# Performance work log

Measured on AMD Instinct MI355X. Metric: run time of the kernel, lower is better.

## Reference

```python
import jax, jax.numpy as jnp
import numpy as np

K = 8  # knn_graph(k=8, loop=True): self-loop kept, so self is among the k nearest


def knn_idx(x, k):
    # x: [N, F]. Pairwise squared distances via the expansion trick.
    x2 = jnp.sum(x * x, axis=-1)                      # [N]
    d = x2[:, None] + x2[None, :] - 2.0 * (x @ x.T)   # [N, N]
    _, idx = jax.lax.top_k(-d, k)                     # [N, k] nearest (incl. self)
    return idx


def edge_conv(x, idx, W1, b1, W2, b2):
    # PyG EdgeConv: message = nn(cat([x_i, x_j - x_i])), aggr='max'.
    # Every node has exactly k incoming edges, so scatter-max == max over the k axis.
    n, f = x.shape
    k = idx.shape[1]
    xi = x[:, None, :]                                # [N, 1, F] center
    xj = x[idx]                                       # [N, k, F] neighbors (gather)
    e = jnp.concatenate([jnp.broadcast_to(xi, (n, k, f)), xj - xi], axis=-1)  # [N,k,2F]
    h = jax.nn.relu(e @ W1 + b1) @ W2 + b2            # [N, k, out]
    return jnp.max(h, axis=1)                         # [N, out]


def setup_inputs() -> dict:
    key = jax.random.key(0)
    ks = jax.random.split(key, 9)
    B, N, F = 2, 4096, 3
    H0, H1, OUT = 64, 128, 256

    def lin(kw, fan_in, fan_out):
        bound = 1.0 / np.sqrt(fan_in)
        kw1, kw2 = jax.random.split(kw)
        W = jax.random.uniform(kw1, (fan_in, fan_out), jnp.float32, -bound, bound)
        b = jax.random.uniform(kw2, (fan_out,), jnp.float32, -bound, bound)
        return W, b

    W1, b1 = lin(ks[0], 2 * F, H0)
    W2, b2 = lin(ks[1], H0, H1)
    W3, b3 = lin(ks[2], 2 * H1, H1)
    W4, b4 = lin(ks[3], H1, OUT)
    point_cloud = jax.random.normal(ks[4], (B, N, F), jnp.float32)
    return {"point_cloud": point_cloud, "W1": W1, "b1": b1, "W2": W2, "b2": b2,
            "W3": W3, "b3": b3, "W4": W4, "b4": b4}


def reference(point_cloud, W1, b1, W2, b2, W3, b3, W4, b4):
    B, N, F = point_cloud.shape
    pts = point_cloud.reshape(B * N, F)               # knn over ALL B*N points (no batch vec)
    idx = knn_idx(jax.lax.stop_gradient(pts), K)      # [B*N, K]
    x = jax.nn.relu(edge_conv(pts, idx, W1, b1, W2, b2))
    x = edge_conv(x, idx, W3, b3, W4, b4)
    return x.reshape(B, N, -1)
```

## Files before the change

kernel.cpp:

```cpp
#include <hip/hip_runtime.h>

#define NPTS 8192
#define NSLICE 64
#define SLICE_LEN (NPTS / NSLICE)
#define KNN 8
#define SURV_CAP 48
#define TQ 32

typedef short bf16x8 __attribute__((ext_vector_type(8)));
typedef float f32x4 __attribute__((ext_vector_type(4)));

__device__ __forceinline__ unsigned short f2bf(float x) {
  unsigned int u = __float_as_uint(x);
  return (unsigned short)((u + 0x7FFF + ((u >> 16) & 1)) >> 16);
}
__device__ __forceinline__ float bf2f(unsigned short s) {
  return __uint_as_float(((unsigned int)s) << 16);
}

__device__ __forceinline__ float dist_exact(float qx, float qy, float qz,
                                            float q2, float px, float py,
                                            float pz, float p2) {
#pragma clang fp contract(off)
  float dot = __fmaf_rn(qz, pz, __fmaf_rn(qy, py, __fmul_rn(qx, px)));
  float t1 = __fadd_rn(q2, p2);
  return __fadd_rn(t1, __fmul_rn(-2.0f, dot));
}

__device__ __forceinline__ float norm2_exact(float x, float y, float z) {
#pragma clang fp contract(off)
  return __fadd_rn(__fadd_rn(__fmul_rn(x, x), __fmul_rn(y, y)),
                   __fmul_rn(z, z));
}

__device__ __forceinline__ float med3(float a, float b, float c) {
  return __builtin_amdgcn_fmed3f(a, b, c);
}

__device__ __forceinline__ double pack_key(float d, int idx) {
  unsigned int ub = __float_as_uint(d);
  ub ^= (((unsigned int)((int)ub >> 31)) | 0x80000000u);
  unsigned int lo = (ub << 13) | (unsigned int)idx;
  unsigned int hi = 0x3ff00000u | (ub >> 19);
  return __hiloint2double((int)hi, (int)lo);
}

#define KEY_DECL                                                            \
  const double KINF = __longlong_as_double(0x7ff0000000000000LL);           \
  double k0 = KINF, k1 = KINF, k2 = KINF, k3 = KINF, k4 = KINF, k5 = KINF,  \
         k6 = KINF, k7 = KINF;
#define KB1(s)                                                              \
  {                                                                         \
    double mn = fmin(carry, k##s);                                          \
    carry = fmax(carry, k##s);                                              \
    k##s = mn;                                                              \
  }
#define KEY_INSERT(key)                                                     \
  {                                                                         \
    double carry = (key);                                                   \
    KB1(0) KB1(1) KB1(2) KB1(3) KB1(4) KB1(5) KB1(6) KB1(7)                 \
  }

#define VINS(dv)                                                            \
  {                                                                         \
    float dd = (dv);                                                        \
    v7 = med3(dd, v6, v7);                                                  \
    v6 = med3(dd, v5, v6);                                                  \
    v5 = med3(dd, v4, v5);                                                  \
    v4 = med3(dd, v3, v4);                                                  \
    v3 = med3(dd, v2, v2 < dd ? dd : v3);                                   \
    v2 = med3(dd, v1, v2);                                                  \
    v1 = med3(dd, v0, v1);                                                  \
    v0 = fminf(dd, v0);                                                     \
  }

#undef VINS
#define VINS(dv)                                                            \
  {                                                                         \
    float dd = (dv);                                                        \
    v7 = med3(dd, v6, v7);                                                  \
    v6 = med3(dd, v5, v6);                                                  \
    v5 = med3(dd, v4, v5);                                                  \
    v4 = med3(dd, v3, v4);                                                  \
    v3 = med3(dd, v2, v3);                                                  \
    v2 = med3(dd, v1, v2);                                                  \
    v1 = med3(dd, v0, v1);                                                  \
    v0 = fminf(dd, v0);                                                     \
  }

#define VDECL                                                               \
  const float FINF = __uint_as_float(0x7f800000u);                          \
  float v0 = FINF, v1 = FINF, v2 = FINF, v3 = FINF, v4 = FINF, v5 = FINF,   \
        v6 = FINF, v7 = FINF;

#define VINS2(dv)                                                           \
  {                                                                         \
    float dd = (dv);                                                        \
    s1 = med3(dd, s0, s1);                                                  \
    s0 = fminf(dd, s0);                                                     \
  }

__global__ __launch_bounds__(256) void prep_kernel(
    const float* __restrict__ W4, const float* __restrict__ pts,
    unsigned short* __restrict__ W4ht, unsigned short* __restrict__ W4lt,
    float4* __restrict__ pts4) {
  const int id = blockIdx.x * 256 + threadIdx.x;
  const int k = id >> 8, c = id & 255;
  float v = W4[k * 256 + c];
  unsigned short hi = f2bf(v);
  unsigned short lo = f2bf(v - bf2f(hi));
  W4ht[c * 128 + k] = hi;
  W4lt[c * 128 + k] = lo;
  if (id < NPTS) {
    float x = pts[id * 3 + 0];
    float y = pts[id * 3 + 1];
    float z = pts[id * 3 + 2];
    pts4[id] = make_float4(x, y, z, norm2_exact(x, y, z));
  }
}

__global__ __launch_bounds__(256) void knn_vals_kernel(
    const float4* __restrict__ pts4, float* __restrict__ part_v) {
  __shared__ float4 sp[SLICE_LEN];
  const int t = threadIdx.x;
  const int q = blockIdx.x * 256 + t;
  const int jbase = blockIdx.y * SLICE_LEN;
  for (int p = t; p < SLICE_LEN; p += 256) sp[p] = pts4[jbase + p];
  __syncthreads();
  const float4 qp = pts4[q];
  const float qx = qp.x, qy = qp.y, qz = qp.z, q2 = qp.w;
  const float FINF = __uint_as_float(0x7f800000u);
  float s0 = FINF, s1 = FINF;
  for (int p = 0; p < SLICE_LEN; p += 8) {
    float4 c0 = sp[p + 0];
    float4 c1 = sp[p + 1];
    float4 c2 = sp[p + 2];
    float4 c3 = sp[p + 3];
    float4 c4 = sp[p + 4];
    float4 c5 = sp[p + 5];
    float4 c6 = sp[p + 6];
    float4 c7 = sp[p + 7];
    float d0 = dist_exact(qx, qy, qz, q2, c0.x, c0.y, c0.z, c0.w);
    float d1 = dist_exact(qx, qy, qz, q2, c1.x, c1.y, c1.z, c1.w);
    float d2 = dist_exact(qx, qy, qz, q2, c2.x, c2.y, c2.z, c2.w);
    float d3 = dist_exact(qx, qy, qz, q2, c3.x, c3.y, c3.z, c3.w);
    float d4 = dist_exact(qx, qy, qz, q2, c4.x, c4.y, c4.z, c4.w);
    float d5 = dist_exact(qx, qy, qz, q2, c5.x, c5.y, c5.z, c5.w);
    float d6 = dist_exact(qx, qy, qz, q2, c6.x, c6.y, c6.z, c6.w);
    float d7 = dist_exact(qx, qy, qz, q2, c7.x, c7.y, c7.z, c7.w);
    VINS2(d0);
    VINS2(d1);
    VINS2(d2);
    VINS2(d3);
    VINS2(d4);
    VINS2(d5);
    VINS2(d6);
    VINS2(d7);
  }
  float* o = &part_v[(size_t)(blockIdx.y * 2) * NPTS + q];
  o[0 * NPTS] = s0;
  o[1 * NPTS] = s1;
}

__global__ __launch_bounds__(256) void knn_thresh_kernel(
    const float* __restrict__ part_v, float* __restrict__ thr,
    unsigned long long* __restrict__ mask) {
  __shared__ float v8s[TQ][8][9];
  __shared__ float smin[TQ][65];
  const int t = threadIdx.x;
  const int lq = t >> 3, c = t & 7;
  const int q = blockIdx.x * TQ + lq;
  {
    VDECL;
#pragma unroll
    for (int s8 = 0; s8 < 8; ++s8) {
      const int s = c * 8 + s8;
      const float* col = &part_v[(size_t)(s * 2) * NPTS + q];
      float a0 = col[0 * (size_t)NPTS];
      float a1 = col[1 * (size_t)NPTS];
      smin[lq][s] = a0;
      VINS(a0);
      VINS(a1);
    }
    v8s[lq][c][0] = v0;
    v8s[lq][c][1] = v1;
    v8s[lq][c][2] = v2;
    v8s[lq][c][3] = v3;
    v8s[lq][c][4] = v4;
    v8s[lq][c][5] = v5;
    v8s[lq][c][6] = v6;
    v8s[lq][c][7] = v7;
  }
  __syncthreads();
  if (c == 0) {
    VDECL;
#pragma unroll
    for (int s = 0; s < 8; ++s) {
      VINS(v8s[lq][s][0]);
      VINS(v8s[lq][s][1]);
      VINS(v8s[lq][s][2]);
      VINS(v8s[lq][s][3]);
      VINS(v8s[lq][s][4]);
      VINS(v8s[lq][s][5]);
      VINS(v8s[lq][s][6]);
      VINS(v8s[lq][s][7]);
    }
    const float tcol = v7 + fabsf(v7) * 4e-5f + 1e-20f;
    const float tmask = v7 + fabsf(v7) * 8e-5f + 2e-20f;
    unsigned long long mk = 0;
#pragma unroll
    for (int s = 0; s < NSLICE; ++s) {
      if (smin[lq][s] <= tmask) mk |= (1ull << s);
    }
    thr[q] = tcol;
    mask[q] = mk;
  }
}

__global__ __launch_bounds__(256) void knn_collect_kernel(
    const float4* __restrict__ pts4, const float* __restrict__ thr,
    const unsigned long long* __restrict__ mask, int* __restrict__ nbr) {
  __shared__ double keybuf[4][SURV_CAP];
  __shared__ int scnt[4];
  const int t = threadIdx.x;
  const int wv = t >> 6;
  const int lane = t & 63;
  const int q = blockIdx.x * 4 + wv;
  if (lane == 0) scnt[wv] = 0;
  __syncthreads();
  const float4 qp = pts4[q];
  const float qx = qp.x, qy = qp.y, qz = qp.z, q2 = qp.w;
  const float thrq = thr[q];
  unsigned long long m = mask[q];
  while (m) {
    const int s = (int)__ffsll(m) - 1;
    m &= m - 1;
    const int base = s * SLICE_LEN;
#pragma unroll
    for (int r = 0; r < SLICE_LEN / 64; ++r) {
      const int j = base + r * 64 + lane;
      const float4 cp = pts4[j];
      const float d = dist_exact(qx, qy, qz, q2, cp.x, cp.y, cp.z, cp.w);
      if (d <= thrq) {
        int slot = atomicAdd(&scnt[wv], 1);
        if (slot < SURV_CAP) keybuf[wv][slot] = pack_key(d, j);
      }
    }
  }
  __syncthreads();
  if (lane == 0) {
    int c = scnt[wv];
    if (c > SURV_CAP) c = SURV_CAP;
    KEY_DECL;
    for (int u = 0; u < c; ++u) {
      KEY_INSERT(keybuf[wv][u]);
    }
    int* o = &nbr[q * KNN];
    o[0] = __double2loint(k0) & 0x1fff;
    o[1] = __double2loint(k1) & 0x1fff;
    o[2] = __double2loint(k2) & 0x1fff;
    o[3] = __double2loint(k3) & 0x1fff;
    o[4] = __double2loint(k4) & 0x1fff;
    o[5] = __double2loint(k5) & 0x1fff;
    o[6] = __double2loint(k6) & 0x1fff;
    o[7] = __double2loint(k7) & 0x1fff;
  }
}

__global__ __launch_bounds__(256) void gemm1_fused_kernel(
    const float* __restrict__ pts, const int* __restrict__ nbr,
    const float* __restrict__ W1, const float* __restrict__ b1,
    const float* __restrict__ W2, const float* __restrict__ b2,
    float* __restrict__ y) {
  __shared__ float es[64][6];
  __shared__ float W1s[6][64];
  __shared__ float b1s[64];
  __shared__ float As[64][64];
  __shared__ float Bs[64][64];
  const int t = threadIdx.x;
  const int rowBase = blockIdx.y * 64;
  const int colBase = blockIdx.x * 64;

  for (int idx = t; idx < 384; idx += 256) W1s[idx >> 6][idx & 63] = W1[idx];
  if (t < 64) b1s[t] = b1[t];
  {
    int cq = t & 15, kr = t >> 4;
#pragma unroll
    for (int it = 0; it < 4; ++it) {
      int k = it * 16 + kr;
      *(float4*)&Bs[k][cq * 4] =
          *(const float4*)&W2[(size_t)k * 128 + colBase + cq * 4];
    }
  }
  if (t < 64) {
    int e = rowBase + t;
    int i = e >> 3;
    int j = nbr[e];
    float xi0 = pts[i * 3], xi1 = pts[i * 3 + 1], xi2 = pts[i * 3 + 2];
    es[t][0] = xi0;
    es[t][1] = xi1;
    es[t][2] = xi2;
    es[t][3] = pts[j * 3] - xi0;
    es[t][4] = pts[j * 3 + 1] - xi1;
    es[t][5] = pts[j * 3 + 2] - xi2;
  }
  __syncthreads();

  {
    const int e = t & 63, k0 = (t >> 6) * 16;
    const float f0 = es[e][0], f1 = es[e][1], f2 = es[e][2];
    const float f3 = es[e][3], f4 = es[e][4], f5 = es[e][5];
#pragma unroll
    for (int k = 0; k < 16; ++k) {
      int c = k0 + k;
      float v = b1s[c];
      v = fmaf(f0, W1s[0][c], v);
      v = fmaf(f1, W1s[1][c], v);
      v = fmaf(f2, W1s[2][c], v);
      v = fmaf(f3, W1s[3][c], v);
      v = fmaf(f4, W1s[4][c], v);
      v = fmaf(f5, W1s[5][c], v);
      As[c][e] = fmaxf(v, 0.0f);
    }
  }
  __syncthreads();

  const int tx = t & 15, ty = t >> 4;
  float acc[4][4] = {};
#pragma unroll 8
  for (int k = 0; k < 64; ++k) {
    float4 a = *(const float4*)&As[k][ty * 4];
    float4 b = *(const float4*)&Bs[k][tx * 4];
    const float ar[4] = {a.x, a.y, a.z, a.w};
    const float br[4] = {b.x, b.y, b.z, b.w};
#pragma unroll
    for (int i = 0; i < 4; ++i)
#pragma unroll
      for (int jj = 0; jj < 4; ++jj)
        acc[i][jj] = fmaf(ar[i], br[jj], acc[i][jj]);
  }
  __syncthreads();

  float* Mx = &As[0][0];
#pragma unroll
  for (int jj = 0; jj < 4; ++jj) {
    float m =
        fmaxf(fmaxf(acc[0][jj], acc[1][jj]), fmaxf(acc[2][jj], acc[3][jj]));
    Mx[ty * 64 + tx * 4 + jj] = m;
  }
  __syncthreads();
  if (t < 128) {
    int p = t >> 4, cq = t & 15;
    int c = cq * 4;
    float4 o;
    float* oa = (float*)&o;
#pragma unroll
    for (int jj = 0; jj < 4; ++jj) {
      float v = fmaxf(Mx[(2 * p) * 64 + c + jj], Mx[(2 * p + 1) * 64 + c + jj]);
      v += b2[colBase + c + jj];
      oa[jj] = fmaxf(v, 0.0f);
    }
    *(float4*)&y[(size_t)(blockIdx.y * 8 + p) * 128 + colBase + c] = o;
  }
}

__global__ __launch_bounds__(256) void gemm_ac_kernel(
    const float* __restrict__ A, const float* __restrict__ W3,
    const float* __restrict__ bias, float* __restrict__ out) {
  __shared__ float As[64][64];
  __shared__ float Bs[64][64];
  const int t = threadIdx.x;
  const int tx = t & 15, ty = t >> 4;
  const int rowBase = blockIdx.y * 64;
  const int colBase = blockIdx.x * 64;
  const float4* A4 = (const float4*)A;
  float acc[4][4] = {};
  const int K = 128, Nglob = 256;

  for (int k0 = 0; k0 < K; k0 += 64) {
#pragma unroll
    for (int it = 0; it < 4; ++it) {
      int idx = it * 256 + t;
      int row = idx & 63, kq = idx >> 6;
      float4 av = A4[(size_t)(rowBase + row) * (K >> 2) + (k0 >> 2) + kq];
      As[kq * 4 + 0][row] = av.x;
      As[kq * 4 + 1][row] = av.y;
      As[kq * 4 + 2][row] = av.z;
      As[kq * 4 + 3][row] = av.w;
    }
#pragma unroll
    for (int it = 0; it < 4; ++it) {
      int idx = it * 256 + t;
      int cq = idx & 15, kr = idx >> 4;
      const float* src =
          (colBase < 128)
              ? &W3[(size_t)(k0 + kr) * 128 + colBase]
              : &W3[(size_t)(128 + k0 + kr) * 128 + (colBase - 128)];
      float4 bv = *(const float4*)&src[cq * 4];
      *(float4*)&Bs[kr][cq * 4] = bv;
    }
    __syncthreads();
#pragma unroll 8
    for (int k = 0; k < 64; ++k) {
      float4 a = *(const float4*)&As[k][ty * 4];
      float4 b = *(const float4*)&Bs[k][tx * 4];
      const float ar[4] = {a.x, a.y, a.z, a.w};
      const float br[4] = {b.x, b.y, b.z, b.w};
#pragma unroll
      for (int i = 0; i < 4; ++i)
#pragma unroll
        for (int jj = 0; jj < 4; ++jj)
          acc[i][jj] = fmaf(ar[i], br[jj], acc[i][jj]);
    }
    __syncthreads();
  }

#pragma unroll
  for (int i = 0; i < 4; ++i) {
    float4 o;
    float* oa = (float*)&o;
#pragma unroll
    for (int jj = 0; jj < 4; ++jj) {
      float v = acc[i][jj];
      int cg = colBase + tx * 4 + jj;
      if (cg < 128) v += bias[cg];
      oa[jj] = v;
    }
    *(float4*)&out[(size_t)(rowBase + ty * 4 + i) * Nglob + colBase + tx * 4] =
        o;
  }
}

__global__ __launch_bounds__(256) void gemm2_mfma_kernel(
    const float* __restrict__ AC, const int* __restrict__ nbr,
    const unsigned short* __restrict__ W4ht,
    const unsigned short* __restrict__ W4lt, const float* __restrict__ b4,
    float* __restrict__ out) {
  __shared__ unsigned short H2h[128 * 40];
  __shared__ unsigned short H2l[128 * 40];
  __shared__ unsigned short Wth[128 * 40];
  __shared__ unsigned short Wtl[128 * 40];
  const int t = threadIdx.x;
  const int rowBase = blockIdx.y * 128;
  const int colBase = blockIdx.x * 128;
  const int eloc = t >> 1, hh = t & 1;
  const int kb = hh * 16;
  const int edge = rowBase + eloc;
  const int ip = edge >> 3;
  const int jp = nbr[edge];
  const float* ai_p = AC + (size_t)ip * 256;
  const float* ci_p = ai_p + 128;
  const float* cj_p = AC + (size_t)jp * 256 + 128;
  const int lane = t & 63;
  const int w = t >> 6;
  const int q = lane >> 4;
  const int nidx = lane & 15;

  f32x4 acc[2][8];
#pragma unroll
  for (int mt = 0; mt < 2; ++mt)
#pragma unroll
    for (int nt = 0; nt < 8; ++nt) acc[mt][nt] = (f32x4){0.f, 0.f, 0.f, 0.f};

  for (int p = 0; p < 4; ++p) {
    const int k0 = p * 32;
    {
      float h2[16];
      const float4* a4 = (const float4*)(ai_p + k0 + kb);
      const float4* c4 = (const float4*)(ci_p + k0 + kb);
      const float4* d4 = (const float4*)(cj_p + k0 + kb);
#pragma unroll
      for (int u = 0; u < 4; ++u) {
        float4 a = a4[u], c = c4[u], d = d4[u];
        h2[u * 4 + 0] = fmaxf(a.x + d.x - c.x, 0.f);
        h2[u * 4 + 1] = fmaxf(a.y + d.y - c.y, 0.f);
        h2[u * 4 + 2] = fmaxf(a.z + d.z - c.z, 0.f);
        h2[u * 4 + 3] = fmaxf(a.w + d.w - c.w, 0.f);
      }
      unsigned int hp[8], lp[8];
#pragma unroll
      for (int u = 0; u < 8; ++u) {
        unsigned short h0 = f2bf(h2[2 * u]), h1 = f2bf(h2[2 * u + 1]);
        hp[u] = (unsigned int)h0 | ((unsigned int)h1 << 16);
        unsigned short l0 = f2bf(h2[2 * u] - bf2f(h0));
        unsigned short l1 = f2bf(h2[2 * u + 1] - bf2f(h1));
        lp[u] = (unsigned int)l0 | ((unsigned int)l1 << 16);
      }
      *(uint4*)&H2h[eloc * 40 + kb] = make_uint4(hp[0], hp[1], hp[2], hp[3]);
      *(uint4*)&H2h[eloc * 40 + kb + 8] =
          make_uint4(hp[4], hp[5], hp[6], hp[7]);
      *(uint4*)&H2l[eloc * 40 + kb] = make_uint4(lp[0], lp[1], lp[2], lp[3]);
      *(uint4*)&H2l[eloc * 40 + kb + 8] =
          make_uint4(lp[4], lp[5], lp[6], lp[7]);
    }
    {
      const size_t src = (size_t)(colBase + eloc) * 128 + k0 + kb;
      *(uint4*)&Wth[eloc * 40 + kb] = *(const uint4*)&W4ht[src];
      *(uint4*)&Wth[eloc * 40 + kb + 8] = *(const uint4*)&W4ht[src + 8];
      *(uint4*)&Wtl[eloc * 40 + kb] = *(const uint4*)&W4lt[src];
      *(uint4*)&Wtl[eloc * 40 + kb + 8] = *(const uint4*)&W4lt[src + 8];
    }
    __syncthreads();
    bf16x8 ah[2], al[2];
#pragma unroll
    for (int mt = 0; mt < 2; ++mt) {
      int row = w * 32 + mt * 16 + nidx;
      ah[mt] = *(const bf16x8*)&H2h[row * 40 + q * 8];
      al[mt] = *(const bf16x8*)&H2l[row * 40 + q * 8];
    }
#pragma unroll
    for (int nt = 0; nt < 8; ++nt) {
      int col = nt * 16 + nidx;
      bf16x8 bh = *(const bf16x8*)&Wth[col * 40 + q * 8];
      bf16x8 bl = *(const bf16x8*)&Wtl[col * 40 + q * 8];
#pragma unroll
      for (int mt = 0; mt < 2; ++mt) {
        acc[mt][nt] = __builtin_amdgcn_mfma_f32_16x16x32_bf16(
            ah[mt], bh, acc[mt][nt], 0, 0, 0);
        acc[mt][nt] = __builtin_amdgcn_mfma_f32_16x16x32_bf16(
            ah[mt], bl, acc[mt][nt], 0, 0, 0);
        acc[mt][nt] = __builtin_amdgcn_mfma_f32_16x16x32_bf16(
            al[mt], bh, acc[mt][nt], 0, 0, 0);
      }
    }
    __syncthreads();
  }

#pragma unroll
  for (int mt = 0; mt < 2; ++mt) {
    const int ebase = rowBase + w * 32 + mt * 16;
    const int pt0 = ebase >> 3;
#pragma unroll
    for (int nt = 0; nt < 8; ++nt) {
      f32x4 a = acc[mt][nt];
      float m = fmaxf(fmaxf(a[0], a[1]), fmaxf(a[2], a[3]));
      float o = fmaxf(m, __shfl_xor(m, 16, 64));
      int cg = colBase + nt * 16 + nidx;
      if (q == 0) {
        out[(size_t)pt0 * 256 + cg] = o + b4[cg];
      } else if (q == 2) {
        out[(size_t)(pt0 + 1) * 256 + cg] = o + b4[cg];
      }
    }
  }
}

extern "C" void kernel_launch(void* const* d_in, const int* in_sizes, int n_in,
                              void* d_out, int out_size, void* d_ws,
                              size_t ws_size, hipStream_t stream) {
  const float* pts = (const float*)d_in[0];
  const float* W1 = (const float*)d_in[1];
  const float* b1 = (const float*)d_in[2];
  const float* W2 = (const float*)d_in[3];
  const float* b2 = (const float*)d_in[4];
  const float* W3 = (const float*)d_in[5];
  const float* b3 = (const float*)d_in[6];
  const float* W4 = (const float*)d_in[7];
  const float* b4 = (const float*)d_in[8];
  float* out = (float*)d_out;

  float* w = (float*)d_ws;
  float* part_v = w;
  float* thr = w + 4194304;
  int* nbr = (int*)(w + 4202496);
  float* y = w + 4268032;
  unsigned long long* mask = (unsigned long long*)(w + 5316608);
  unsigned short* W4ht = (unsigned short*)(w + 5332992);
  unsigned short* W4lt = (unsigned short*)(w + 5349376);
  float4* pts4 = (float4*)(w + 5365760);
  float* AC = w;

  prep_kernel<<<128, 256, 0, stream>>>(W4, pts, W4ht, W4lt, pts4);

  knn_vals_kernel<<<dim3(32, NSLICE), 256, 0, stream>>>(pts4, part_v);
  knn_thresh_kernel<<<NPTS / TQ, 256, 0, stream>>>(part_v, thr, mask);
  knn_collect_kernel<<<2048, 256, 0, stream>>>(pts4, thr, mask, nbr);

  gemm1_fused_kernel<<<dim3(2, 1024), 256, 0, stream>>>(pts, nbr, W1, b1, W2,
                                                        b2, y);

  gemm_ac_kernel<<<dim3(4, 128), 256, 0, stream>>>(y, W3, b3, AC);
  gemm2_mfma_kernel<<<dim3(2, 512), 256, 0, stream>>>(AC, nbr, W4ht, W4lt, b4,
                                                      out);
}
```

Baseline: 161.7 us.

## Replace FP32 FMA GEMM in first EdgeConv with split-bf16 MFMA

The second layer of the first EdgeConv MLP moves from a scalar FP32 4x4 register-tiled GEMM to bf16 MFMA 16x16x32 instructions. Both the activation and the W2 weights are split into hi/lo bf16 parts, and three cross products are summed to approximate FP32 accuracy. W2 is converted and transposed once in the prep kernel, and the max over the 8 neighbours is done with a wave shuffle instead of a shared-memory pass. This aims to cut the FP32 ALU cost of the gemm1 stage, at the price of extra conversion work and a small accuracy loss from dropping the lo×lo term.

```diff
diff --git a/kernel.cpp b/kernel.cpp
--- a/kernel.cpp
+++ b/kernel.cpp
@@ -61,20 +61,6 @@
     KB1(0) KB1(1) KB1(2) KB1(3) KB1(4) KB1(5) KB1(6) KB1(7)                 \
   }
 
-#define VINS(dv)                                                            \
-  {                                                                         \
-    float dd = (dv);                                                        \
-    v7 = med3(dd, v6, v7);                                                  \
-    v6 = med3(dd, v5, v6);                                                  \
-    v5 = med3(dd, v4, v5);                                                  \
-    v4 = med3(dd, v3, v4);                                                  \
-    v3 = med3(dd, v2, v2 < dd ? dd : v3);                                   \
-    v2 = med3(dd, v1, v2);                                                  \
-    v1 = med3(dd, v0, v1);                                                  \
-    v0 = fminf(dd, v0);                                                     \
-  }
-
-#undef VINS
 #define VINS(dv)                                                            \
   {                                                                         \
     float dd = (dv);                                                        \
@@ -102,8 +88,9 @@
 
 __global__ __launch_bounds__(256) void prep_kernel(
     const float* __restrict__ W4, const float* __restrict__ pts,
-    unsigned short* __restrict__ W4ht, unsigned short* __restrict__ W4lt,
-    float4* __restrict__ pts4) {
+    const float* __restrict__ W2, unsigned short* __restrict__ W4ht,
+    unsigned short* __restrict__ W4lt, unsigned short* __restrict__ W2th,
+    unsigned short* __restrict__ W2tl, float4* __restrict__ pts4) {
   const int id = blockIdx.x * 256 + threadIdx.x;
   const int k = id >> 8, c = id & 255;
   float v = W4[k * 256 + c];
@@ -116,6 +103,11 @@
     float y = pts[id * 3 + 1];
     float z = pts[id * 3 + 2];
     pts4[id] = make_float4(x, y, z, norm2_exact(x, y, z));
+    const int kk = id >> 7, cc = id & 127;
+    float v2 = W2[kk * 128 + cc];
+    unsigned short h2 = f2bf(v2);
+    W2th[cc * 64 + kk] = h2;
+    W2tl[cc * 64 + kk] = f2bf(v2 - bf2f(h2));
   }
 }
 
@@ -270,13 +262,16 @@
 __global__ __launch_bounds__(256) void gemm1_fused_kernel(
     const float* __restrict__ pts, const int* __restrict__ nbr,
     const float* __restrict__ W1, const float* __restrict__ b1,
-    const float* __restrict__ W2, const float* __restrict__ b2,
+    const unsigned short* __restrict__ W2th,
+    const unsigned short* __restrict__ W2tl, const float* __restrict__ b2,
     float* __restrict__ y) {
   __shared__ float es[64][6];
   __shared__ float W1s[6][64];
   __shared__ float b1s[64];
-  __shared__ float As[64][64];
-  __shared__ float Bs[64][64];
+  __shared__ unsigned short H1h[64 * 72];
+  __shared__ unsigned short H1l[64 * 72];
+  __shared__ unsigned short Wth[64 * 72];
+  __shared__ unsigned short Wtl[64 * 72];
   const int t = threadIdx.x;
   const int rowBase = blockIdx.y * 64;
   const int colBase = blockIdx.x * 64;
@@ -284,13 +279,12 @@
   for (int idx = t; idx < 384; idx += 256) W1s[idx >> 6][idx & 63] = W1[idx];
   if (t < 64) b1s[t] = b1[t];
   {
-    int cq = t & 15, kr = t >> 4;
-#pragma unroll
-    for (int it = 0; it < 4; ++it) {
-      int k = it * 16 + kr;
-      *(float4*)&Bs[k][cq * 4] =
-          *(const float4*)&W2[(size_t)k * 128 + colBase + cq * 4];
-    }
+    const int colloc = t >> 2, kq = (t & 3) * 16;
+    const size_t src = (size_t)(colBase + colloc) * 64 + kq;
+    *(uint4*)&Wth[colloc * 72 + kq] = *(const uint4*)&W2th[src];
+    *(uint4*)&Wth[colloc * 72 + kq + 8] = *(const uint4*)&W2th[src + 8];
+    *(uint4*)&Wtl[colloc * 72 + kq] = *(const uint4*)&W2tl[src];
+    *(uint4*)&Wtl[colloc * 72 + kq + 8] = *(const uint4*)&W2tl[src + 8];
   }
   if (t < 64) {
     int e = rowBase + t;
@@ -310,6 +304,7 @@
     const int e = t & 63, k0 = (t >> 6) * 16;
     const float f0 = es[e][0], f1 = es[e][1], f2 = es[e][2];
     const float f3 = es[e][3], f4 = es[e][4], f5 = es[e][5];
+    float h[16];
 #pragma unroll
     for (int k = 0; k < 16; ++k) {
       int c = k0 + k;
@@ -320,47 +315,62 @@
       v = fmaf(f3, W1s[3][c], v);
       v = fmaf(f4, W1s[4][c], v);
       v = fmaf(f5, W1s[5][c], v);
-      As[c][e] = fmaxf(v, 0.0f);
-    }
+      h[k] = fmaxf(v, 0.0f);
+    }
+    unsigned int hp[8], lp[8];
+#pragma unroll
+    for (int u = 0; u < 8; ++u) {
+      unsigned short h0 = f2bf(h[2 * u]), h1 = f2bf(h[2 * u + 1]);
+      hp[u] = (unsigned int)h0 | ((unsigned int)h1 << 16);
+      unsigned short l0 = f2bf(h[2 * u] - bf2f(h0));
+      unsigned short l1 = f2bf(h[2 * u + 1] - bf2f(h1));
+      lp[u] = (unsigned int)l0 | ((unsigned int)l1 << 16);
+    }
+    *(uint4*)&H1h[e * 72 + k0] = make_uint4(hp[0], hp[1], hp[2], hp[3]);
+    *(uint4*)&H1h[e * 72 + k0 + 8] = make_uint4(hp[4], hp[5], hp[6], hp[7]);
+    *(uint4*)&H1l[e * 72 + k0] = make_uint4(lp[0], lp[1], lp[2], lp[3]);
+    *(uint4*)&H1l[e * 72 + k0 + 8] = make_uint4(lp[4], lp[5], lp[6], lp[7]);
   }
   __syncthreads();
 
-  const int tx = t & 15, ty = t >> 4;
-  float acc[4][4] = {};
-#pragma unroll 8
-  for (int k = 0; k < 64; ++k) {
-    float4 a = *(const float4*)&As[k][ty * 4];
-    float4 b = *(const float4*)&Bs[k][tx * 4];
-    const float ar[4] = {a.x, a.y, a.z, a.w};
-    const float br[4] = {b.x, b.y, b.z, b.w};
-#pragma unroll
-    for (int i = 0; i < 4; ++i)
-#pragma unroll
-      for (int jj = 0; jj < 4; ++jj)
-        acc[i][jj] = fmaf(ar[i], br[jj], acc[i][jj]);
-  }
-  __syncthreads();
-
-  float* Mx = &As[0][0];
-#pragma unroll
-  for (int jj = 0; jj < 4; ++jj) {
-    float m =
-        fmaxf(fmaxf(acc[0][jj], acc[1][jj]), fmaxf(acc[2][jj], acc[3][jj]));
-    Mx[ty * 64 + tx * 4 + jj] = m;
-  }
-  __syncthreads();
-  if (t < 128) {
-    int p = t >> 4, cq = t & 15;
-    int c = cq * 4;
-    float4 o;
-    float* oa = (float*)&o;
-#pragma unroll
-    for (int jj = 0; jj < 4; ++jj) {
-      float v = fmaxf(Mx[(2 * p) * 64 + c + jj], Mx[(2 * p + 1) * 64 + c + jj]);
-      v += b2[colBase + c + jj];
-      oa[jj] = fmaxf(v, 0.0f);
-    }
-    *(float4*)&y[(size_t)(blockIdx.y * 8 + p) * 128 + colBase + c] = o;
+  const int lane = t & 63, w = t >> 6;
+  const int qq = lane >> 4, nidx = lane & 15;
+  f32x4 acc[4];
+#pragma unroll
+  for (int nt = 0; nt < 4; ++nt) acc[nt] = (f32x4){0.f, 0.f, 0.f, 0.f};
+  bf16x8 ah0, ah1, al0, al1;
+  {
+    const int row = w * 16 + nidx;
+    ah0 = *(const bf16x8*)&H1h[row * 72 + qq * 8];
+    ah1 = *(const bf16x8*)&H1h[row * 72 + 32 + qq * 8];
+    al0 = *(const bf16x8*)&H1l[row * 72 + qq * 8];
+    al1 = *(const bf16x8*)&H1l[row * 72 + 32 + qq * 8];
+  }
+#pragma unroll
+  for (int nt = 0; nt < 4; ++nt) {
+    const int col = nt * 16 + nidx;
+    bf16x8 bh0 = *(const bf16x8*)&Wth[col * 72 + qq * 8];
+    bf16x8 bh1 = *(const bf16x8*)&Wth[col * 72 + 32 + qq * 8];
+    bf16x8 bl0 = *(const bf16x8*)&Wtl[col * 72 + qq * 8];
+    bf16x8 bl1 = *(const bf16x8*)&Wtl[col * 72 + 32 + qq * 8];
+    acc[nt] = __builtin_amdgcn_mfma_f32_16x16x32_bf16(ah0, bh0, acc[nt], 0, 0, 0);
+    acc[nt] = __builtin_amdgcn_mfma_f32_16x16x32_bf16(ah1, bh1, acc[nt], 0, 0, 0);
+    acc[nt] = __builtin_amdgcn_mfma_f32_16x16x32_bf16(ah0, bl0, acc[nt], 0, 0, 0);
+    acc[nt] = __builtin_amdgcn_mfma_f32_16x16x32_bf16(ah1, bl1, acc[nt], 0, 0, 0);
+    acc[nt] = __builtin_amdgcn_mfma_f32_16x16x32_bf16(al0, bh0, acc[nt], 0, 0, 0);
+    acc[nt] = __builtin_amdgcn_mfma_f32_16x16x32_bf16(al1, bh1, acc[nt], 0, 0, 0);
+  }
+
+  const int pt = blockIdx.y * 8 + 2 * w + (qq >> 1);
+#pragma unroll
+  for (int nt = 0; nt < 4; ++nt) {
+    f32x4 a = acc[nt];
+    float m = fmaxf(fmaxf(a[0], a[1]), fmaxf(a[2], a[3]));
+    float o = fmaxf(m, __shfl_xor(m, 16, 64));
+    if ((qq & 1) == 0) {
+      int cg = colBase + nt * 16 + nidx;
+      y[(size_t)pt * 128 + cg] = fmaxf(o + b2[cg], 0.0f);
+    }
   }
 }
 
@@ -568,16 +578,19 @@
   unsigned short* W4ht = (unsigned short*)(w + 5332992);
   unsigned short* W4lt = (unsigned short*)(w + 5349376);
   float4* pts4 = (float4*)(w + 5365760);
+  unsigned short* W2th = (unsigned short*)(w + 5398528);
+  unsigned short* W2tl = (unsigned short*)(w + 5402624);
   float* AC = w;
 
-  prep_kernel<<<128, 256, 0, stream>>>(W4, pts, W4ht, W4lt, pts4);
+  prep_kernel<<<128, 256, 0, stream>>>(W4, pts, W2, W4ht, W4lt, W2th, W2tl,
+                                       pts4);
 
   knn_vals_kernel<<<dim3(32, NSLICE), 256, 0, stream>>>(pts4, part_v);
   knn_thresh_kernel<<<NPTS / TQ, 256, 0, stream>>>(part_v, thr, mask);
   knn_collect_kernel<<<2048, 256, 0, stream>>>(pts4, thr, mask, nbr);
 
-  gemm1_fused_kernel<<<dim3(2, 1024), 256, 0, stream>>>(pts, nbr, W1, b1, W2,
-                                                        b2, y);
+  gemm1_fused_kernel<<<dim3(2, 1024), 256, 0, stream>>>(pts, nbr, W1, b1,
+                                                        W2th, W2tl, b2, y);
 
   gemm_ac_kernel<<<dim3(4, 128), 256, 0, stream>>>(y, W3, b3, AC);
   gemm2_mfma_kernel<<<dim3(2, 512), 256, 0, stream>>>(AC, nbr, W4ht, W4lt, b4,
```

Result: faster. 157.1 us (-2.9%).
